# Optimization experiments

Measured on AMD Instinct MI355X. Metric: run time of the kernel, lower is better.

## Reference

```python
import jax, jax.numpy as jnp
import numpy as np

B, S, D = 2, 2048, 1024
H, HD = 16, 64

def setup_inputs() -> dict:
    key = jax.random.key(0)
    k1, k2, k3 = jax.random.split(key, 3)
    x = jax.random.normal(k1, (B, S, D), dtype=jnp.float32)
    w_qkv = jax.random.normal(k2, (3 * D, D), dtype=jnp.float32) * (D ** -0.5)
    w_out = jax.random.normal(k3, (D, D), dtype=jnp.float32) * (D ** -0.5)
    return {"x": x, "w_qkv": w_qkv, "w_out": w_out}

def reference(x, w_qkv, w_out):
    scale = HD ** -0.5
    # qkv projection: torch Linear applies x @ W.T
    qkv = jnp.einsum('bsd,ed->bse', x, w_qkv)            # [B,S,3D]
    qkv = qkv.reshape(B, S, 3, H, HD)
    q, k, v = qkv[:, :, 0], qkv[:, :, 1], qkv[:, :, 2]   # [B,S,H,HD]
    # scores: explicit matmul-softmax-matmul (unfused, as in source)
    scores = jnp.einsum('bqhd,bkhd->bhqk', q, k) * scale  # [B,H,S,S]
    attn = jax.nn.softmax(scores, axis=-1)
    out = jnp.einsum('bhqk,bkhd->bqhd', attn, v)          # [B,S,H,HD]
    out = out.reshape(B, S, D)
    return jnp.einsum('bsd,ed->bse', out, w_out)
```

## Files before the change

kernel.cpp:

```cpp
#include <hip/hip_runtime.h>
#include <hip/hip_bf16.h>
#include <math.h>

#define B_ 2
#define S_ 2048
#define D_ 1024
#define H_ 16
#define HD_ 64

typedef short bf16x8 __attribute__((ext_vector_type(8)));
typedef short bf16x4 __attribute__((ext_vector_type(4)));
typedef float f32x4 __attribute__((ext_vector_type(4)));

#define MFMA32(a, b, c) __builtin_amdgcn_mfma_f32_16x16x32_bf16(a, b, c, 0, 0, 0)
#define MFMA16(a, b, c) __builtin_amdgcn_mfma_f32_16x16x16bf16_1k(a, b, c, 0, 0, 0)

static __device__ __forceinline__ unsigned short f2bf(float f) {
    union { float f; unsigned u; } v = {f};
    return (unsigned short)((v.u + 0x7fffu + ((v.u >> 16) & 1u)) >> 16);
}

static __device__ __forceinline__ unsigned pk2bf(float a, float b) {
    __hip_bfloat162 h = __float22bfloat162_rn(make_float2(a, b));
    unsigned r;
    __builtin_memcpy(&r, &h, 4);
    return r;
}

static __device__ __forceinline__ void gl2lds16(const void* g, void* l) {
    __builtin_amdgcn_global_load_lds((const __attribute__((address_space(1))) unsigned int*)g,
                                     (__attribute__((address_space(3))) unsigned int*)l,
                                     16, 0, 0);
}

static __device__ __forceinline__ bf16x8 scaleQ(bf16x8 v, float s) {
    union { bf16x8 v; unsigned u[4]; } a, r;
    a.v = v;
    #pragma unroll
    for (int i = 0; i < 4; ++i) {
        float lo = __uint_as_float(a.u[i] << 16);
        float hi = __uint_as_float(a.u[i] & 0xffff0000u);
        r.u[i] = pk2bf(lo * s, hi * s);
    }
    return r.v;
}

__global__ __launch_bounds__(256) void cvt_all(const float* __restrict__ x,
                                               const float* __restrict__ wq,
                                               const float* __restrict__ wo,
                                               unsigned short* __restrict__ xb,
                                               unsigned short* __restrict__ wqb,
                                               unsigned short* __restrict__ wob) {
    const int N0 = 1048576, N1 = 786432, N2 = 262144;
    int stride = gridDim.x * blockDim.x;
    for (int i = blockIdx.x * blockDim.x + threadIdx.x; i < N0 + N1 + N2; i += stride) {
        const float4* src; ushort4* dst; int j;
        if (i < N0)            { src = (const float4*)x;  dst = (ushort4*)xb;  j = i; }
        else if (i < N0 + N1)  { src = (const float4*)wq; dst = (ushort4*)wqb; j = i - N0; }
        else                   { src = (const float4*)wo; dst = (ushort4*)wob; j = i - N0 - N1; }
        float4 v = src[j];
        ushort4 o;
        o.x = f2bf(v.x); o.y = f2bf(v.y); o.z = f2bf(v.z); o.w = f2bf(v.w);
        dst[j] = o;
    }
}

template <int BM, int BN>
__global__ __launch_bounds__(256, 4) void gemm_nt_b(const unsigned short* __restrict__ A,
                                                    const unsigned short* __restrict__ Bm,
                                                    void* __restrict__ Cout,
                                                    unsigned short* __restrict__ vtout,
                                                    int M, int N, int K, int c_bf16) {
    constexpr int BK = 64;
    constexpr int MI = BM / 32;
    constexpr int NI = BN / 32;
    constexpr int ASEG = BM / 8;
    constexpr int SEGS = (BM + BN) / 8;
    __shared__ unsigned short As[BM * BK];
    __shared__ unsigned short Bs[BN * BK];

    const int tid = threadIdx.x;
    const int wave = tid >> 6, lane = tid & 63;
    const int m16 = lane & 15, quad = lane >> 4;
    const int wrow = (wave >> 1) * (BM / 2);
    const int wcol = (wave & 1) * (BN / 2);
    const int row0 = blockIdx.y * BM, col0 = blockIdx.x * BN;

    const int lr8 = lane >> 3;
    const int lsrc = (lane & 7) ^ lr8;

    const int ka = (quad ^ (m16 & 7)) * 8;

    f32x4 acc[MI][NI] = {};

    const int nk = K / BK;
    for (int kk = 0; kk < nk; ++kk) {
        __syncthreads();
        for (int s = wave; s < SEGS; s += 4) {
            if (s < ASEG) {
                gl2lds16(&A[(size_t)(row0 + s * 8 + lr8) * K + kk * BK + lsrc * 8],
                         &As[s * 8 * BK]);
            } else {
                int t = s - ASEG;
                gl2lds16(&Bm[(size_t)(col0 + t * 8 + lr8) * K + kk * BK + lsrc * 8],
                         &Bs[t * 8 * BK]);
            }
        }
        __asm__ volatile("s_waitcnt vmcnt(0)" ::: "memory");
        __syncthreads();

        #pragma unroll
        for (int kh = 0; kh < 2; ++kh) {
            bf16x8 af[MI], bfr[NI];
            #pragma unroll
            for (int mi = 0; mi < MI; ++mi)
                af[mi] = *(const bf16x8*)&As[((wrow + mi * 16 + m16) * BK + ka) ^ (kh * 32)];
            #pragma unroll
            for (int ni = 0; ni < NI; ++ni)
                bfr[ni] = *(const bf16x8*)&Bs[((wcol + ni * 16 + m16) * BK + ka) ^ (kh * 32)];
            #pragma unroll
            for (int mi = 0; mi < MI; ++mi)
                #pragma unroll
                for (int ni = 0; ni < NI; ++ni)
                    acc[mi][ni] = MFMA32(af[mi], bfr[ni], acc[mi][ni]);
        }
    }

    if (vtout != nullptr && col0 >= 2 * D_) {
        #pragma unroll
        for (int mi = 0; mi < MI; ++mi) {
            int srow = row0 + wrow + mi * 16 + quad * 4;
            int bb = srow >> 11;
            int s = srow & (S_ - 1);
            #pragma unroll
            for (int ni = 0; ni < NI; ++ni) {
                int hd = col0 + wcol + ni * 16 + m16 - 2 * D_;
                ushort4 v4;
                v4.x = f2bf(acc[mi][ni][0]);
                v4.y = f2bf(acc[mi][ni][1]);
                v4.z = f2bf(acc[mi][ni][2]);
                v4.w = f2bf(acc[mi][ni][3]);
                *(ushort4*)&vtout[((size_t)(bb * 16 + (hd >> 6)) * 64 + (hd & 63)) * S_ + s] = v4;
            }
        }
        return;
    }

    #pragma unroll
    for (int mi = 0; mi < MI; ++mi) {
        #pragma unroll
        for (int r = 0; r < 4; ++r) {
            size_t grow = row0 + wrow + mi * 16 + quad * 4 + r;
            #pragma unroll
            for (int ni = 0; ni < NI; ++ni) {
                size_t gcol = col0 + wcol + ni * 16 + m16;
                if (c_bf16)
                    ((unsigned short*)Cout)[grow * N + gcol] = f2bf(acc[mi][ni][r]);
                else
                    ((float*)Cout)[grow * N + gcol] = acc[mi][ni][r];
            }
        }
    }
}

__global__ __launch_bounds__(512, 4) void attn_mfma(const unsigned short* __restrict__ qkv,
                                                    const unsigned short* __restrict__ vt,
                                                    unsigned short* __restrict__ out) {
    __shared__ unsigned short L[2][16384];

    const int id = blockIdx.x;
    const int bh = ((id >> 3) & 3) * 8 + (id & 7);
    const int b = bh >> 4, h = bh & 15;
    const int q0 = (id >> 5) * 128;

    const int tid = threadIdx.x;
    const int wave = tid >> 6, lane = tid & 63;
    const int grp = wave >> 2;
    const int qw = wave & 3;
    const int m16 = lane & 15, quad = lane >> 4;

    const float QS = 0.125f * 1.44269504089f;

    bf16x8 qf0[2], qf1[2];
    #pragma unroll
    for (int g = 0; g < 2; ++g) {
        const unsigned short* qrow =
            qkv + ((size_t)b * S_ + q0 + qw * 32 + g * 16 + m16) * (3 * D_) + h * HD_;
        qf0[g] = scaleQ(*(const bf16x8*)(qrow + quad * 8), QS);
        qf1[g] = scaleQ(*(const bf16x8*)(qrow + 32 + quad * 8), QS);
    }

    f32x4 o[2][4] = {};
    f32x4 ol[2] = {};
    const f32x4 zf = {};
    const bf16x4 onesf = {(short)0x3F80, (short)0x3F80, (short)0x3F80, (short)0x3F80};

    const unsigned short* kbase = qkv + (size_t)b * S_ * 3 * D_ + D_ + h * HD_;
    const unsigned short* vtbase = vt + (size_t)bh * 64 * S_;

    const int lr8 = lane >> 3;
    const int lsrc = (lane & 7) ^ lr8;

    const int kaddr0 = m16 * 64 + ((quad ^ (m16 & 7)) * 8);
    const int kaddr1 = kaddr0 ^ 32;
    int va[4];
    #pragma unroll
    for (int nt = 0; nt < 4; ++nt) {
        int kc = nt * 2 + (quad >> 1);
        va[nt] = m16 * 64 + ((kc ^ (m16 & 7)) * 8) + (quad & 1) * 4;
    }

    auto issueDMA = [&](int pair, int buf) {
        const int mat = wave >> 1;
        const int tt = pair * 2 + (mat >> 1);
        unsigned short* dstb = &L[buf][mat * 4096];
        if ((mat & 1) == 0) {
            const unsigned short* kt = kbase + (size_t)tt * 64 * (3 * D_);
            #pragma unroll
            for (int i = 0; i < 4; ++i) {
                int gi = (wave & 1) * 4 + i;
                gl2lds16(kt + (size_t)(gi * 8 + lr8) * (3 * D_) + lsrc * 8,
                         dstb + gi * 512);
            }
        } else {
            const unsigned short* vtt = vtbase + tt * 64;
            #pragma unroll
            for (int i = 0; i < 4; ++i) {
                int gi = (wave & 1) * 4 + i;
                gl2lds16(vtt + (size_t)(gi * 8 + lr8) * S_ + lsrc * 8,
                         dstb + gi * 512);
            }
        }
    };

    issueDMA(0, 0);
    __asm__ volatile("s_waitcnt vmcnt(0)" ::: "memory");
    __syncthreads();
    issueDMA(1, 1);

    for (int s = 0; s < 16; ++s) {
        const int buf = s & 1;
        const unsigned short* Kp = &L[buf][grp * 8192];
        const unsigned short* Vp = Kp + 4096;

        bf16x4 pf[2][4];
        #pragma unroll
        for (int nt = 0; nt < 4; ++nt) {
            bf16x8 kf0 = *(const bf16x8*)&Kp[kaddr0 + nt * 1024];
            bf16x8 kf1 = *(const bf16x8*)&Kp[kaddr1 + nt * 1024];
            #pragma unroll
            for (int g = 0; g < 2; ++g) {
                f32x4 z = MFMA32(kf0, qf0[g], zf);
                z = MFMA32(kf1, qf1[g], z);
                float p0 = __builtin_amdgcn_exp2f(z[0]);
                float p1 = __builtin_amdgcn_exp2f(z[1]);
                float p2 = __builtin_amdgcn_exp2f(z[2]);
                float p3 = __builtin_amdgcn_exp2f(z[3]);
                union { unsigned u[2]; bf16x4 v; } pk;
                pk.u[0] = pk2bf(p0, p1);
                pk.u[1] = pk2bf(p2, p3);
                pf[g][nt] = pk.v;
                ol[g] = MFMA16(pf[g][nt], onesf, ol[g]);
            }
        }

        __builtin_amdgcn_s_setprio(1);
        #pragma unroll
        for (int nt = 0; nt < 4; ++nt)
            #pragma unroll
            for (int dt = 0; dt < 4; ++dt) {
                bf16x4 vf = *(const bf16x4*)&Vp[va[nt] + dt * 1024];
                o[0][dt] = MFMA16(pf[0][nt], vf, o[0][dt]);
                o[1][dt] = MFMA16(pf[1][nt], vf, o[1][dt]);
            }
        __builtin_amdgcn_s_setprio(0);

        __asm__ volatile("s_waitcnt vmcnt(0)" ::: "memory");
        __syncthreads();
        if (s + 2 < 16) issueDMA(s + 2, buf);
    }

    float* M = (float*)&L[0][0];
    const int mb = (qw * 64 + lane) * 44;
    if (grp == 1) {
        #pragma unroll
        for (int g = 0; g < 2; ++g) {
            #pragma unroll
            for (int dt = 0; dt < 4; ++dt)
                *(f32x4*)&M[mb + (g * 4 + dt) * 4] = o[g][dt];
            *(f32x4*)&M[mb + 32 + g * 4] = ol[g];
        }
    }
    __syncthreads();
    if (grp == 0) {
        #pragma unroll
        for (int g = 0; g < 2; ++g) {
            #pragma unroll
            for (int dt = 0; dt < 4; ++dt)
                o[g][dt] += *(const f32x4*)&M[mb + (g * 4 + dt) * 4];
            ol[g] += *(const f32x4*)&M[mb + 32 + g * 4];
        }
        #pragma unroll
        for (int g = 0; g < 2; ++g)
            #pragma unroll
            for (int r = 0; r < 4; ++r) {
                float inv = 1.f / ol[g][r];
                size_t row = (size_t)b * S_ + q0 + qw * 32 + g * 16 + quad * 4 + r;
                unsigned short* op = out + row * D_ + h * HD_;
                #pragma unroll
                for (int dt = 0; dt < 4; ++dt)
                    op[dt * 16 + m16] = f2bf(o[g][dt][r] * inv);
            }
    }
}

extern "C" void kernel_launch(void* const* d_in, const int* in_sizes, int n_in,
                              void* d_out, int out_size, void* d_ws, size_t ws_size,
                              hipStream_t stream) {
    const float* x     = (const float*)d_in[0];
    const float* w_qkv = (const float*)d_in[1];
    const float* w_out = (const float*)d_in[2];
    float* out = (float*)d_out;

    const size_t n_x = (size_t)B_ * S_ * D_;
    const size_t n_wqkv = (size_t)3 * D_ * D_;
    const size_t n_wout = (size_t)D_ * D_;

    unsigned short* xb    = (unsigned short*)d_ws;
    unsigned short* wqkvb = xb + n_x;
    unsigned short* woutb = wqkvb + n_wqkv;
    unsigned short* qkvb  = woutb + n_wout;
    unsigned short* attnb = qkvb + (size_t)B_ * S_ * 3 * D_;
    unsigned short* vtb   = attnb + n_x;

    dim3 blk(256);

    cvt_all<<<2048, blk, 0, stream>>>(x, w_qkv, w_out, xb, wqkvb, woutb);

    gemm_nt_b<128, 128><<<dim3(3 * D_ / 128, B_ * S_ / 128), blk, 0, stream>>>(
        xb, wqkvb, qkvb, vtb, B_ * S_, 3 * D_, D_, 1);

    attn_mfma<<<512, dim3(512), 0, stream>>>(qkvb, vtb, attnb);

    gemm_nt_b<64, 64><<<dim3(D_ / 64, B_ * S_ / 64), blk, 0, stream>>>(
        attnb, woutb, out, nullptr, B_ * S_, D_, D_, 0);
}
```

Measured before the change: 177.8 us.

## Triple-buffer GEMM LDS tiles with async prefetch two stages ahead

```diff
diff --git a/kernel.cpp b/kernel.cpp
--- a/kernel.cpp
+++ b/kernel.cpp
@@ -65,19 +65,18 @@
     }
 }
 
-template <int BM, int BN>
-__global__ __launch_bounds__(256, 4) void gemm_nt_b(const unsigned short* __restrict__ A,
+template <int BM, int BN, int BK>
+__global__ __launch_bounds__(256, 3) void gemm_nt_b(const unsigned short* __restrict__ A,
                                                     const unsigned short* __restrict__ Bm,
                                                     void* __restrict__ Cout,
                                                     unsigned short* __restrict__ vtout,
                                                     int M, int N, int K, int c_bf16) {
-    constexpr int BK = 64;
     constexpr int MI = BM / 32;
     constexpr int NI = BN / 32;
-    constexpr int ASEG = BM / 8;
-    constexpr int SEGS = (BM + BN) / 8;
-    __shared__ unsigned short As[BM * BK];
-    __shared__ unsigned short Bs[BN * BK];
+    constexpr int ASEG = BM * BK / 512;
+    constexpr int SEGS = (BM + BN) * BK / 512;
+    __shared__ __attribute__((aligned(16))) unsigned short As[3][BM * BK];
+    __shared__ __attribute__((aligned(16))) unsigned short Bs[3][BN * BK];
 
     const int tid = threadIdx.x;
     const int wave = tid >> 6, lane = tid & 63;
@@ -88,41 +87,78 @@
 
     const int lr8 = lane >> 3;
     const int lsrc = (lane & 7) ^ lr8;
+    const int lr16 = lane >> 2;
+    const int lk32 = (lane & 3) * 8;
 
     const int ka = (quad ^ (m16 & 7)) * 8;
 
     f32x4 acc[MI][NI] = {};
 
-    const int nk = K / BK;
-    for (int kk = 0; kk < nk; ++kk) {
-        __syncthreads();
-        for (int s = wave; s < SEGS; s += 4) {
+    auto stage = [&](int kk, int buf) {
+        #pragma unroll
+        for (int i = 0; i < SEGS / 4; ++i) {
+            int s = wave + i * 4;
+            const unsigned short* src;
+            unsigned short* dst;
             if (s < ASEG) {
-                gl2lds16(&A[(size_t)(row0 + s * 8 + lr8) * K + kk * BK + lsrc * 8],
-                         &As[s * 8 * BK]);
+                if constexpr (BK == 32)
+                    src = &A[(size_t)(row0 + s * 16 + lr16) * K + kk * BK + lk32];
+                else
+                    src = &A[(size_t)(row0 + s * 8 + lr8) * K + kk * BK + lsrc * 8];
+                dst = &As[buf][s * 512];
             } else {
                 int t = s - ASEG;
-                gl2lds16(&Bm[(size_t)(col0 + t * 8 + lr8) * K + kk * BK + lsrc * 8],
-                         &Bs[t * 8 * BK]);
-            }
-        }
-        __asm__ volatile("s_waitcnt vmcnt(0)" ::: "memory");
-        __syncthreads();
-
-        #pragma unroll
-        for (int kh = 0; kh < 2; ++kh) {
+                if constexpr (BK == 32)
+                    src = &Bm[(size_t)(col0 + t * 16 + lr16) * K + kk * BK + lk32];
+                else
+                    src = &Bm[(size_t)(col0 + t * 8 + lr8) * K + kk * BK + lsrc * 8];
+                dst = &Bs[buf][t * 512];
+            }
+            gl2lds16(src, dst);
+        }
+    };
+
+    const int nk = K / BK;
+    stage(0, 0);
+    stage(1, 1);
+
+    for (int kk = 0; kk < nk; ++kk) {
+        if (kk + 1 < nk)
+            __asm__ volatile("s_waitcnt vmcnt(4)\n\ts_barrier" ::: "memory");
+        else
+            __asm__ volatile("s_waitcnt vmcnt(0)\n\ts_barrier" ::: "memory");
+        if (kk + 2 < nk) stage(kk + 2, (kk + 2) % 3);
+        const int buf = kk % 3;
+
+        if constexpr (BK == 32) {
             bf16x8 af[MI], bfr[NI];
             #pragma unroll
             for (int mi = 0; mi < MI; ++mi)
-                af[mi] = *(const bf16x8*)&As[((wrow + mi * 16 + m16) * BK + ka) ^ (kh * 32)];
+                af[mi] = *(const bf16x8*)&As[buf][(wrow + mi * 16 + m16) * BK + quad * 8];
             #pragma unroll
             for (int ni = 0; ni < NI; ++ni)
-                bfr[ni] = *(const bf16x8*)&Bs[((wcol + ni * 16 + m16) * BK + ka) ^ (kh * 32)];
+                bfr[ni] = *(const bf16x8*)&Bs[buf][(wcol + ni * 16 + m16) * BK + quad * 8];
             #pragma unroll
             for (int mi = 0; mi < MI; ++mi)
                 #pragma unroll
                 for (int ni = 0; ni < NI; ++ni)
                     acc[mi][ni] = MFMA32(af[mi], bfr[ni], acc[mi][ni]);
+        } else {
+            #pragma unroll
+            for (int kh = 0; kh < 2; ++kh) {
+                bf16x8 af[MI], bfr[NI];
+                #pragma unroll
+                for (int mi = 0; mi < MI; ++mi)
+                    af[mi] = *(const bf16x8*)&As[buf][((wrow + mi * 16 + m16) * BK + ka) ^ (kh * 32)];
+                #pragma unroll
+                for (int ni = 0; ni < NI; ++ni)
+                    bfr[ni] = *(const bf16x8*)&Bs[buf][((wcol + ni * 16 + m16) * BK + ka) ^ (kh * 32)];
+                #pragma unroll
+                for (int mi = 0; mi < MI; ++mi)
+                    #pragma unroll
+                    for (int ni = 0; ni < NI; ++ni)
+                        acc[mi][ni] = MFMA32(af[mi], bfr[ni], acc[mi][ni]);
+            }
         }
     }
 
@@ -337,11 +373,11 @@
 
     cvt_all<<<2048, blk, 0, stream>>>(x, w_qkv, w_out, xb, wqkvb, woutb);
 
-    gemm_nt_b<128, 128><<<dim3(3 * D_ / 128, B_ * S_ / 128), blk, 0, stream>>>(
+    gemm_nt_b<128, 128, 32><<<dim3(3 * D_ / 128, B_ * S_ / 128), blk, 0, stream>>>(
         xb, wqkvb, qkvb, vtb, B_ * S_, 3 * D_, D_, 1);
 
     attn_mfma<<<512, dim3(512), 0, stream>>>(qkvb, vtb, attnb);
 
-    gemm_nt_b<64, 64><<<dim3(D_ / 64, B_ * S_ / 64), blk, 0, stream>>>(
+    gemm_nt_b<64, 64, 64><<<dim3(D_ / 64, B_ * S_ / 64), blk, 0, stream>>>(
         attnb, woutb, out, nullptr, B_ * S_, D_, D_, 0);
 }
```

After: 184.7 us. 1.04x slower.

## Add 256x256 eight-phase pipelined QKV GEMM with double-buffered LDS staging

Applied to the files above, without the earlier changes.

```diff
diff --git a/kernel.cpp b/kernel.cpp
--- a/kernel.cpp
+++ b/kernel.cpp
@@ -65,11 +65,121 @@
     }
 }
 
+__global__ __launch_bounds__(512, 2) void gemm_qkv_8ph(const unsigned short* __restrict__ A,
+                                                       const unsigned short* __restrict__ Bm,
+                                                       unsigned short* __restrict__ qkv,
+                                                       unsigned short* __restrict__ vt) {
+    constexpr int Kd = 1024, Nd = 3072;
+    __shared__ unsigned short Lsh[65536];
+
+    const int tid = threadIdx.x;
+    const int wave = tid >> 6, lane = tid & 63;
+    const int m16 = lane & 15, quad = lane >> 4;
+    const int wr = wave >> 2, wc = wave & 3;
+    const int row0 = blockIdx.y * 256, col0 = blockIdx.x * 256;
+
+    f32x4 acc[8][4] = {};
+
+    auto stageHalf = [&](int kt, int j) {
+        const int slot = kt & 1;
+        const unsigned short* src = (j < 2) ? A : Bm;
+        const int base0 = ((j < 2) ? row0 : col0) + (j & 1) * 128;
+        unsigned short* dst = &Lsh[slot * 32768 + (j >> 1) * 16384 + (j & 1) * 8192];
+        const int kc = kt * 64;
+        #pragma unroll
+        for (int l = 0; l < 2; ++l) {
+            int seg = l * 512 + tid;
+            int r = seg >> 3, sl = seg & 7;
+            gl2lds16(src + (size_t)(base0 + r) * Kd + kc + ((sl ^ (r & 7)) * 8),
+                     dst + (l * 512 + wave * 64) * 8);
+        }
+    };
+
+    #pragma unroll
+    for (int j = 0; j < 4; ++j) stageHalf(0, j);
+    __asm__ volatile("s_waitcnt vmcnt(0)" ::: "memory");
+    __syncthreads();
+
+    for (int it = 0; it < 8; ++it) {
+        bf16x8 af[4][2];
+        #pragma unroll
+        for (int ph = 0; ph < 8; ++ph) {
+            const int slot = ph >> 2;
+            const int miH = (ph >> 1) & 1, niH = ph & 1;
+            const unsigned short* Ah = &Lsh[slot * 32768 + wr * 8192];
+            const unsigned short* Bh = &Lsh[slot * 32768 + 16384 + (wc >> 1) * 8192];
+
+            if (niH == 0) {
+                #pragma unroll
+                for (int i2 = 0; i2 < 4; ++i2)
+                    #pragma unroll
+                    for (int kh = 0; kh < 2; ++kh)
+                        af[i2][kh] = *(const bf16x8*)&Ah[((miH * 4 + i2) * 16 + m16) * 64 +
+                                                         (((kh * 4 + quad) ^ (m16 & 7)) * 8)];
+            }
+            bf16x8 bf[2][2];
+            #pragma unroll
+            for (int j2 = 0; j2 < 2; ++j2)
+                #pragma unroll
+                for (int kh = 0; kh < 2; ++kh)
+                    bf[j2][kh] = *(const bf16x8*)&Bh[((wc & 1) * 64 + (niH * 2 + j2) * 16 + m16) * 64 +
+                                                     (((kh * 4 + quad) ^ (m16 & 7)) * 8)];
+
+            const int T = 2 * it + ((ph < 4) ? 1 : 2);
+            if (T < 16) stageHalf(T, ph & 3);
+
+            if ((ph & 3) == 3) __asm__ volatile("s_waitcnt vmcnt(0)" ::: "memory");
+            __builtin_amdgcn_s_barrier();
+            __asm__ volatile("s_waitcnt lgkmcnt(0)" ::: "memory");
+            __builtin_amdgcn_sched_barrier(0);
+            __builtin_amdgcn_s_setprio(1);
+            #pragma unroll
+            for (int i2 = 0; i2 < 4; ++i2)
+                #pragma unroll
+                for (int j2 = 0; j2 < 2; ++j2) {
+                    const int mi = miH * 4 + i2, ni = niH * 2 + j2;
+                    acc[mi][ni] = MFMA32(af[i2][0], bf[j2][0], acc[mi][ni]);
+                    acc[mi][ni] = MFMA32(af[i2][1], bf[j2][1], acc[mi][ni]);
+                }
+            __builtin_amdgcn_s_setprio(0);
+            __builtin_amdgcn_s_barrier();
+        }
+    }
+
+    if (col0 >= 2 * D_) {
+        #pragma unroll
+        for (int mi = 0; mi < 8; ++mi) {
+            int srow = row0 + wr * 128 + mi * 16 + quad * 4;
+            int bb = srow >> 11;
+            int s = srow & (S_ - 1);
+            #pragma unroll
+            for (int ni = 0; ni < 4; ++ni) {
+                int hd = col0 + wc * 64 + ni * 16 + m16 - 2 * D_;
+                ushort4 v4;
+                v4.x = f2bf(acc[mi][ni][0]);
+                v4.y = f2bf(acc[mi][ni][1]);
+                v4.z = f2bf(acc[mi][ni][2]);
+                v4.w = f2bf(acc[mi][ni][3]);
+                *(ushort4*)&vt[((size_t)(bb * 16 + (hd >> 6)) * 64 + (hd & 63)) * S_ + s] = v4;
+            }
+        }
+    } else {
+        #pragma unroll
+        for (int mi = 0; mi < 8; ++mi)
+            #pragma unroll
+            for (int r = 0; r < 4; ++r) {
+                size_t grow = row0 + wr * 128 + mi * 16 + quad * 4 + r;
+                #pragma unroll
+                for (int ni = 0; ni < 4; ++ni)
+                    qkv[grow * Nd + col0 + wc * 64 + ni * 16 + m16] = f2bf(acc[mi][ni][r]);
+            }
+    }
+}
+
 template <int BM, int BN>
 __global__ __launch_bounds__(256, 4) void gemm_nt_b(const unsigned short* __restrict__ A,
                                                     const unsigned short* __restrict__ Bm,
                                                     void* __restrict__ Cout,
-                                                    unsigned short* __restrict__ vtout,
                                                     int M, int N, int K, int c_bf16) {
     constexpr int BK = 64;
     constexpr int MI = BM / 32;
@@ -124,26 +234,6 @@
                 for (int ni = 0; ni < NI; ++ni)
                     acc[mi][ni] = MFMA32(af[mi], bfr[ni], acc[mi][ni]);
         }
-    }
-
-    if (vtout != nullptr && col0 >= 2 * D_) {
-        #pragma unroll
-        for (int mi = 0; mi < MI; ++mi) {
-            int srow = row0 + wrow + mi * 16 + quad * 4;
-            int bb = srow >> 11;
-            int s = srow & (S_ - 1);
-            #pragma unroll
-            for (int ni = 0; ni < NI; ++ni) {
-                int hd = col0 + wcol + ni * 16 + m16 - 2 * D_;
-                ushort4 v4;
-                v4.x = f2bf(acc[mi][ni][0]);
-                v4.y = f2bf(acc[mi][ni][1]);
-                v4.z = f2bf(acc[mi][ni][2]);
-                v4.w = f2bf(acc[mi][ni][3]);
-                *(ushort4*)&vtout[((size_t)(bb * 16 + (hd >> 6)) * 64 + (hd & 63)) * S_ + s] = v4;
-            }
-        }
-        return;
     }
 
     #pragma unroll
@@ -337,11 +427,11 @@
 
     cvt_all<<<2048, blk, 0, stream>>>(x, w_qkv, w_out, xb, wqkvb, woutb);
 
-    gemm_nt_b<128, 128><<<dim3(3 * D_ / 128, B_ * S_ / 128), blk, 0, stream>>>(
-        xb, wqkvb, qkvb, vtb, B_ * S_, 3 * D_, D_, 1);
+    gemm_qkv_8ph<<<dim3(3 * D_ / 256, B_ * S_ / 256), dim3(512), 0, stream>>>(
+        xb, wqkvb, qkvb, vtb);
 
     attn_mfma<<<512, dim3(512), 0, stream>>>(qkvb, vtb, attnb);
 
     gemm_nt_b<64, 64><<<dim3(D_ / 64, B_ * S_ / 64), blk, 0, stream>>>(
-        attnb, woutb, out, nullptr, B_ * S_, D_, D_, 0);
-}
+        attnb, woutb, out, B_ * S_, D_, D_, 0);
+}
```

New measurement: 187.0 us. 1.05x slower.
